# Kernel tuning notes

Measured on AMD Instinct MI355X. Metric: run time of the kernel, lower is better.

The kernel has to match this reference:

```python
import jax, jax.numpy as jnp
import numpy as np
import math

N_HEADS = 12
HEAD_DIM = 64
D_MODEL = 768
BATCH = 2
SEQ = 2048
GRID = 46  # num_patches_per_side


def _rope_1d(x, pos, dim):
    # x: (B,S,H,dim), pos: (S,) int -> rotary embedding along last dim
    inv_freq = 1.0 / (10000.0 ** (jnp.arange(0, dim, 2, dtype=jnp.float32) / dim))  # (dim/2,)
    ang = pos.astype(jnp.float32)[:, None] * inv_freq  # (S, dim/2)
    cos = jnp.concatenate([jnp.cos(ang), jnp.cos(ang)], axis=-1)[None, :, None, :]
    sin = jnp.concatenate([jnp.sin(ang), jnp.sin(ang)], axis=-1)[None, :, None, :]
    x1, x2 = jnp.split(x, 2, axis=-1)
    rot = jnp.concatenate([-x2, x1], axis=-1)
    return x * cos.astype(x.dtype) + rot * sin.astype(x.dtype)


def _rope_2d(x, row_ids, col_ids):
    # 2D RoPE: first half of head_dim rotated by row position, second half by column position
    half = x.shape[-1] // 2
    xr = _rope_1d(x[..., :half], row_ids, half)
    xc = _rope_1d(x[..., half:], col_ids, half)
    return jnp.concatenate([xr, xc], axis=-1)


def setup_inputs() -> dict:
    key = jax.random.key(0)
    ks = jax.random.split(key, 7)
    scale = 1.0 / math.sqrt(D_MODEL)
    return {
        "x": jax.random.normal(ks[0], (BATCH, SEQ, D_MODEL), dtype=jnp.float32),
        "row_ids": jax.random.randint(ks[1], (SEQ,), 0, GRID),
        "col_ids": jax.random.randint(ks[2], (SEQ,), 0, GRID),
        "Wq": jax.random.normal(ks[3], (D_MODEL, D_MODEL), dtype=jnp.float32) * scale,
        "Wk": jax.random.normal(ks[4], (D_MODEL, D_MODEL), dtype=jnp.float32) * scale,
        "Wv": jax.random.normal(ks[5], (D_MODEL, D_MODEL), dtype=jnp.float32) * scale,
        "Wo": jax.random.normal(ks[6], (D_MODEL, D_MODEL), dtype=jnp.float32) * scale,
    }


def reference(x, row_ids, col_ids, Wq, Wk, Wv, Wo):
    B, S, _ = x.shape
    # projections (nn.Linear: y = x @ W.T)
    q = (x @ Wq.T).reshape(B, S, N_HEADS, HEAD_DIM)
    k = (x @ Wk.T).reshape(B, S, N_HEADS, HEAD_DIM)
    v = (x @ Wv.T).reshape(B, S, N_HEADS, HEAD_DIM)
    q = _rope_2d(q, row_ids, col_ids)
    k = _rope_2d(k, row_ids, col_ids)
    # (B,H,S,D)
    q = q.transpose(0, 2, 1, 3)
    k = k.transpose(0, 2, 1, 3)
    v = v.transpose(0, 2, 1, 3)
    scale = 1.0 / math.sqrt(HEAD_DIM)
    scores = jnp.einsum('bhqd,bhkd->bhqk', q, k) * scale  # (B,H,S,S)
    causal = jnp.triu(jnp.ones((S, S), dtype=bool), k=1)
    scores = jnp.where(causal, -jnp.inf, scores)
    attn = jax.nn.softmax(scores, axis=-1)
    out = jnp.einsum('bhqk,bhkd->bhqd', attn, v)
    out = out.transpose(0, 2, 1, 3).reshape(B, S, D_MODEL)
    return out @ Wo.T
```

## Files before the change

kernel.cpp:

```cpp
#include <hip/hip_runtime.h>
#include <stdint.h>
#include <stddef.h>

#define DEV __device__ __forceinline__

typedef unsigned short u16;
typedef __attribute__((ext_vector_type(8))) __bf16 bf16x8;
typedef __attribute__((ext_vector_type(4))) float f32x4;
typedef __attribute__((ext_vector_type(8))) unsigned short u16x8;
typedef __attribute__((ext_vector_type(4))) unsigned short u16x4;

DEV u16 f2bf(float f) {
  uint32_t u = __builtin_bit_cast(uint32_t, f);
  u += 0x7fffu + ((u >> 16) & 1u);
  return (u16)(u >> 16);
}
DEV float bf2f(u16 h) {
  uint32_t u = ((uint32_t)h) << 16;
  return __builtin_bit_cast(float, u);
}
DEV f32x4 mfma16(bf16x8 a, bf16x8 b, f32x4 c) {
  return __builtin_amdgcn_mfma_f32_16x16x32_bf16(a, b, c, 0, 0, 0);
}
DEV void ld_lds16(const void* g, void* l) {
  __builtin_amdgcn_global_load_lds((const __attribute__((address_space(1))) void*)g,
                                   (__attribute__((address_space(3))) void*)l, 16, 0, 0);
}

#define Q_SCALE 0.18033688011112042f

__global__ __launch_bounds__(256) void k_cvt_all(const float* __restrict__ x,
                                                 const float* __restrict__ wq,
                                                 const float* __restrict__ wk,
                                                 const float* __restrict__ wv,
                                                 const float* __restrict__ wo,
                                                 u16* __restrict__ dx,
                                                 u16* __restrict__ dqkv,
                                                 u16* __restrict__ dwo) {
  const int bid = blockIdx.x;
  const float* src;
  u16* dst;
  int off;
  if (bid < 3072) {
    src = x; dst = dx; off = bid;
  } else {
    const int t = bid - 3072;
    const int w = t / 576;
    off = t - w * 576;
    src = (w == 0) ? wq : (w == 1) ? wk : (w == 2) ? wv : wo;
    dst = (w < 3) ? (dqkv + (size_t)w * 589824) : dwo;
  }
  const int i = (off * 256 + threadIdx.x) * 4;
  const float4 f = *(const float4*)(src + i);
  u16x4 o;
  o.x = f2bf(f.x); o.y = f2bf(f.y); o.z = f2bf(f.z); o.w = f2bf(f.w);
  *(u16x4*)(dst + i) = o;
}

__global__ __launch_bounds__(256) void k_gemm_qkv(const u16* __restrict__ A,
                                                  const u16* __restrict__ B,
                                                  const int* __restrict__ row_ids,
                                                  const int* __restrict__ col_ids,
                                                  u16* __restrict__ Qh,
                                                  u16* __restrict__ Kh,
                                                  u16* __restrict__ Vt) {
  const int K = 768;
  __shared__ __align__(16) u16 sA[128 * 64];
  __shared__ __align__(16) u16 sB[128 * 64];
  __shared__ int sIds[256];
  const int tid = threadIdx.x;
  const int lane = tid & 63;
  const int wid = tid >> 6;
  const int wm = wid & 1, wn = wid >> 1;
  const int col16 = lane & 15, quad = lane >> 4;
  const int rowBase = blockIdx.y * 128;
  const int colBase = blockIdx.x * 128;
  const int seg_r = lane >> 3;
  const int seg_c = lane & 7;

  f32x4 zero; zero[0] = zero[1] = zero[2] = zero[3] = 0.0f;
  f32x4 acc[4][4];
#pragma unroll
  for (int i = 0; i < 4; ++i)
#pragma unroll
    for (int j = 0; j < 4; ++j) acc[i][j] = zero;

  for (int k0 = 0; k0 < K; k0 += 64) {
#pragma unroll
    for (int c = 0; c < 4; ++c) {
      const int seg = wid * 4 + c;
      ld_lds16(A + (size_t)(rowBase + seg * 8 + seg_r) * K + k0 + seg_c * 8, sA + seg * 512);
      ld_lds16(B + (size_t)(colBase + seg * 8 + seg_r) * K + k0 + seg_c * 8, sB + seg * 512);
    }
    __syncthreads();
#pragma unroll
    for (int kk = 0; kk < 2; ++kk) {
      bf16x8 af[4], bfr[4];
#pragma unroll
      for (int t = 0; t < 4; ++t) {
        af[t]  = *(const bf16x8*)(sA + (wm * 64 + t * 16 + col16) * 64 + kk * 32 + quad * 8);
        bfr[t] = *(const bf16x8*)(sB + (wn * 64 + t * 16 + col16) * 64 + kk * 32 + quad * 8);
      }
#pragma unroll
      for (int tm = 0; tm < 4; ++tm)
#pragma unroll
        for (int tn = 0; tn < 4; ++tn)
          acc[tm][tn] = mfma16(af[tm], bfr[tn], acc[tm][tn]);
    }
    __syncthreads();
  }

  const int bx = blockIdx.x;
  const int type = bx / 6;
  const int h = (bx % 6) * 2 + wn;
  const int bb = rowBase >> 11;
  const int s0 = rowBase & 2047;
  const size_t bh = (size_t)bb * 12 + h;

  if (type < 2) {
    if (tid < 128) {
      sIds[tid] = row_ids[s0 + tid];
      sIds[128 + tid] = col_ids[s0 + tid];
    }
    __syncthreads();
    u16* dst = (type == 0) ? Qh : Kh;
    const float scl = (type == 0) ? Q_SCALE : 1.0f;
    const float invf = exp2f(-(float)col16 * 0.8304820237218406f);
#pragma unroll
    for (int tm = 0; tm < 4; ++tm)
#pragma unroll
      for (int r = 0; r < 4; ++r) {
        const int lrow = wm * 64 + tm * 16 + quad * 4 + r;
        const float aR = (float)sIds[lrow] * invf;
        const float aC = (float)sIds[128 + lrow] * invf;
        const float cR = __cosf(aR), sR = __sinf(aR);
        const float cC = __cosf(aC), sC = __sinf(aC);
        const float x1 = acc[tm][0][r], x2 = acc[tm][1][r];
        const float x3 = acc[tm][2][r], x4 = acc[tm][3][r];
        u16* p = dst + (bh * 2048 + s0 + lrow) * 64;
        p[col16]      = f2bf((x1 * cR - x2 * sR) * scl);
        p[col16 + 16] = f2bf((x2 * cR + x1 * sR) * scl);
        p[col16 + 32] = f2bf((x3 * cC - x4 * sC) * scl);
        p[col16 + 48] = f2bf((x4 * cC + x3 * sC) * scl);
      }
  } else {
#pragma unroll
    for (int tm = 0; tm < 4; ++tm)
#pragma unroll
      for (int tn = 0; tn < 4; ++tn) {
        const int d = tn * 16 + col16;
        const int srow = s0 + wm * 64 + tm * 16 + quad * 4;
        u16x4 o4;
#pragma unroll
        for (int r = 0; r < 4; ++r) o4[r] = f2bf(acc[tm][tn][r]);
        *(u16x4*)(Vt + (bh * 64 + d) * 2048 + srow) = o4;
      }
  }
}

__global__ __launch_bounds__(256, 3) void k_gemm_o(const u16* __restrict__ A,
                                                   const u16* __restrict__ B,
                                                   float* __restrict__ C,
                                                   int N, int K) {
  __shared__ __align__(16) u16 sA[64 * 72];
  __shared__ __align__(16) u16 sB[64 * 72];
  const int tid = threadIdx.x;
  const int lane = tid & 63;
  const int wid = tid >> 6;
  const int col16 = lane & 15, quad = lane >> 4;
  const int wm = wid & 1, wn = wid >> 1;
  const int rowBase = blockIdx.y * 64;
  const int colBase = blockIdx.x * 64;
  const int sr = tid >> 3;
  const int sc8 = (tid & 7) * 8;

  f32x4 zero; zero[0] = zero[1] = zero[2] = zero[3] = 0.0f;
  f32x4 acc[2][2];
  acc[0][0] = zero; acc[0][1] = zero; acc[1][0] = zero; acc[1][1] = zero;

  u16x8 ar[2], br[2];
  auto gload = [&](int k0) {
    ar[0] = *(const u16x8*)(A + (size_t)(rowBase + sr) * K + k0 + sc8);
    ar[1] = *(const u16x8*)(A + (size_t)(rowBase + 32 + sr) * K + k0 + sc8);
    br[0] = *(const u16x8*)(B + (size_t)(colBase + sr) * K + k0 + sc8);
    br[1] = *(const u16x8*)(B + (size_t)(colBase + 32 + sr) * K + k0 + sc8);
  };

  gload(0);
  for (int k0 = 0; k0 < K; k0 += 64) {
    __syncthreads();
    *(u16x8*)&sA[sr * 72 + sc8] = ar[0];
    *(u16x8*)&sA[(32 + sr) * 72 + sc8] = ar[1];
    *(u16x8*)&sB[sr * 72 + sc8] = br[0];
    *(u16x8*)&sB[(32 + sr) * 72 + sc8] = br[1];
    if (k0 + 64 < K) gload(k0 + 64);
    __syncthreads();
#pragma unroll
    for (int kk = 0; kk < 2; ++kk) {
      bf16x8 af[2], bfr[2];
#pragma unroll
      for (int t = 0; t < 2; ++t) {
        af[t]  = *(const bf16x8*)&sA[(wm * 32 + t * 16 + col16) * 72 + kk * 32 + quad * 8];
        bfr[t] = *(const bf16x8*)&sB[(wn * 32 + t * 16 + col16) * 72 + kk * 32 + quad * 8];
      }
#pragma unroll
      for (int tm = 0; tm < 2; ++tm)
#pragma unroll
        for (int tn = 0; tn < 2; ++tn)
          acc[tm][tn] = mfma16(af[tm], bfr[tn], acc[tm][tn]);
    }
  }

#pragma unroll
  for (int tm = 0; tm < 2; ++tm)
#pragma unroll
    for (int tn = 0; tn < 2; ++tn)
#pragma unroll
      for (int r = 0; r < 4; ++r) {
        const int row = rowBase + wm * 32 + tm * 16 + quad * 4 + r;
        const int col = colBase + wn * 32 + tn * 16 + col16;
        C[(size_t)row * N + col] = acc[tm][tn][r];
      }
}

__global__ __launch_bounds__(256, 3) void k_attn(const u16* __restrict__ Qh,
                                                 const u16* __restrict__ Kh,
                                                 const u16* __restrict__ Vt,
                                                 u16* __restrict__ O,
                                                 u16* __restrict__ Opart,
                                                 float* __restrict__ ml) {
  __shared__ __align__(16) u16 sK[2][64 * 72];
  __shared__ __align__(16) u16 sV[2][64 * 72];
  __shared__ __align__(16) u16 sP[4][16 * 72];
  const int tid = threadIdx.x;
  const int lane = tid & 63;
  const int wid = tid >> 6;
  const int col16 = lane & 15;
  const int quad = lane >> 4;
  const int bx = blockIdx.x;
  const int b3 = bx & 7;
  const int r_ = bx >> 3;
  const int g_ = r_ / 40;
  const int u = 39 - (r_ - g_ * 40);
  const int bh = b3 + 8 * g_;
  int qt2, c;
  if (u < 4)       { qt2 = u; c = 0; }
  else if (u < 12) { const int t = u - 4;  qt2 = 4 + (t >> 1); c = t & 1; }
  else if (u < 24) { const int t = u - 12; const int q3 = t / 3; qt2 = 8 + q3; c = t - q3 * 3; }
  else             { const int t = u - 24; qt2 = 12 + (t >> 2); c = t & 3; }
  const int nc = (qt2 >> 2) + 1;
  const int totTiles = 2 * qt2 + 2;
  const int tile0 = c * 8;
  const int ntiles = min(8, totTiles - tile0);
  const int b = bh / 12, h = bh % 12;
  const int qs0 = qt2 * 128 + wid * 16;

  const u16* Qb = Qh + (size_t)bh * (2048 * 64);
  const u16* Kb = Kh + (size_t)bh * (2048 * 64);
  const u16* Vb = Vt + (size_t)bh * (64 * 2048);

  bf16x8 bQ[2][2];
#pragma unroll
  for (int g = 0; g < 2; ++g) {
    const u16* qp = Qb + (size_t)(qs0 + g * 64 + col16) * 64 + quad * 8;
    bQ[g][0] = *(const bf16x8*)qp;
    bQ[g][1] = *(const bf16x8*)(qp + 32);
  }

  f32x4 zero; zero[0] = zero[1] = zero[2] = zero[3] = 0.0f;
  f32x4 o[2][4];
#pragma unroll
  for (int g = 0; g < 2; ++g)
#pragma unroll
    for (int i = 0; i < 4; ++i) o[g][i] = zero;
  float m_r[2] = {-1e30f, -1e30f}, l_r[2] = {0.0f, 0.0f};

  u16* sPw = &sP[wid][0];

  const int sr = tid >> 3;
  const int sc8 = (tid & 7) * 8;
  u16x8 kr[2], vr[2];
  auto gload = [&](int kt) {
#pragma unroll
    for (int i = 0; i < 2; ++i) {
      kr[i] = *(const u16x8*)(Kb + (size_t)(kt + sr + i * 32) * 64 + sc8);
      vr[i] = *(const u16x8*)(Vb + (size_t)(sr + i * 32) * 2048 + kt + sc8);
    }
  };
  auto lwrite = [&](int buf) {
#pragma unroll
    for (int i = 0; i < 2; ++i) {
      *(u16x8*)&sK[buf][(sr + i * 32) * 72 + sc8] = kr[i];
      *(u16x8*)&sV[buf][(sr + i * 32) * 72 + sc8] = vr[i];
    }
  };

  gload(tile0 * 64);
  lwrite(0);
  if (ntiles > 1) gload((tile0 + 1) * 64);
  __syncthreads();

  for (int ki = 0; ki < ntiles; ++ki) {
    const int buf = ki & 1;
    const int kt = (tile0 + ki) * 64;
    if (ki + 1 < ntiles) {
      lwrite(buf ^ 1);
      if (ki + 2 < ntiles) gload((tile0 + ki + 2) * 64);
    }
    bf16x8 ka0[4], ka1[4];
#pragma unroll
    for (int tn = 0; tn < 4; ++tn) {
      const int base = (tn * 16 + col16) * 72 + quad * 8;
      ka0[tn] = *(const bf16x8*)&sK[buf][base];
      ka1[tn] = *(const bf16x8*)&sK[buf][base + 32];
    }
    f32x4 sc[2][4];
#pragma unroll
    for (int tn = 0; tn < 4; ++tn) {
      sc[0][tn] = mfma16(ka1[tn], bQ[0][1], mfma16(ka0[tn], bQ[0][0], zero));
      sc[1][tn] = mfma16(ka1[tn], bQ[1][1], mfma16(ka0[tn], bQ[1][0], zero));
    }
    bf16x8 va0[4], va1[4];
#pragma unroll
    for (int tn = 0; tn < 4; ++tn) {
      const int base = (tn * 16 + col16) * 72 + quad * 8;
      va0[tn] = *(const bf16x8*)&sV[buf][base];
      va1[tn] = *(const bf16x8*)&sV[buf][base + 32];
    }
#pragma unroll
    for (int g = 0; g < 2; ++g) {
      const int qw = qs0 + g * 64;
      if (kt + 63 > qw) {
#pragma unroll
        for (int tn = 0; tn < 4; ++tn)
#pragma unroll
          for (int rr = 0; rr < 4; ++rr)
            if (kt + tn * 16 + quad * 4 + rr > qw + col16) sc[g][tn][rr] = -1e30f;
      }
      float vm = sc[g][0][0];
#pragma unroll
      for (int tn = 0; tn < 4; ++tn)
#pragma unroll
        for (int rr = 0; rr < 4; ++rr) vm = fmaxf(vm, sc[g][tn][rr]);
      vm = fmaxf(vm, __shfl_xor(vm, 16, 64));
      vm = fmaxf(vm, __shfl_xor(vm, 32, 64));
      if (__any(vm > m_r[g])) {
        const float mn = fmaxf(m_r[g], vm);
        const float alpha = exp2f(m_r[g] - mn);
        m_r[g] = mn;
        l_r[g] *= alpha;
#pragma unroll
        for (int t = 0; t < 4; ++t)
#pragma unroll
          for (int rr = 0; rr < 4; ++rr) o[g][t][rr] *= alpha;
      }
      const float mn = m_r[g];
      float rs = 0.0f;
#pragma unroll
      for (int tn = 0; tn < 4; ++tn)
#pragma unroll
        for (int h2 = 0; h2 < 2; ++h2) {
          const float p0 = exp2f(sc[g][tn][2 * h2] - mn);
          const float p1 = exp2f(sc[g][tn][2 * h2 + 1] - mn);
          const uint32_t u0 = __builtin_bit_cast(uint32_t, p0) & 0xffff0000u;
          const uint32_t u1 = __builtin_bit_cast(uint32_t, p1) & 0xffff0000u;
          rs += __builtin_bit_cast(float, u0) + __builtin_bit_cast(float, u1);
          ((uint32_t*)sPw)[col16 * 36 + tn * 8 + quad * 2 + h2] = u1 | (u0 >> 16);
        }
      rs += __shfl_xor(rs, 16, 64);
      rs += __shfl_xor(rs, 32, 64);
      l_r[g] += rs;
      asm volatile("s_waitcnt lgkmcnt(0)" ::: "memory");
      const bf16x8 bP0 = *(const bf16x8*)(sPw + col16 * 72 + quad * 8);
      const bf16x8 bP1 = *(const bf16x8*)(sPw + col16 * 72 + 32 + quad * 8);
#pragma unroll
      for (int tn = 0; tn < 4; ++tn)
        o[g][tn] = mfma16(va1[tn], bP1, mfma16(va0[tn], bP0, o[g][tn]));
    }
    __syncthreads();
  }

  if (nc == 1) {
#pragma unroll
    for (int g = 0; g < 2; ++g) {
      const float invl = 1.0f / l_r[g];
      const size_t row = (size_t)b * 2048 + qs0 + g * 64 + col16;
#pragma unroll
      for (int tn = 0; tn < 4; ++tn)
#pragma unroll
        for (int h2 = 0; h2 < 2; ++h2) {
          const float v0 = o[g][tn][2 * h2] * invl;
          const float v1 = o[g][tn][2 * h2 + 1] * invl;
          const uint32_t w = (uint32_t)f2bf(v0) | ((uint32_t)f2bf(v1) << 16);
          const int col = h * 64 + tn * 16 + quad * 4 + 2 * h2;
          *(uint32_t*)(O + row * 768 + col) = w;
        }
    }
  } else {
#pragma unroll
    for (int g = 0; g < 2; ++g) {
      const int prow = g * 64 + wid * 16 + col16;
      u16* op = Opart + (size_t)bx * 8192 + prow * 64;
#pragma unroll
      for (int tn = 0; tn < 4; ++tn)
#pragma unroll
        for (int h2 = 0; h2 < 2; ++h2) {
          const uint32_t w = (uint32_t)f2bf(o[g][tn][2 * h2]) |
                             ((uint32_t)f2bf(o[g][tn][2 * h2 + 1]) << 16);
          *(uint32_t*)(op + tn * 16 + quad * 4 + 2 * h2) = w;
        }
      if (quad == 0) {
        float* mlp = ml + (size_t)bx * 256;
        mlp[prow] = m_r[g];
        mlp[128 + prow] = l_r[g];
      }
    }
  }
}

__global__ __launch_bounds__(256) void k_combine(const u16* __restrict__ Opart,
                                                 const float* __restrict__ ml,
                                                 u16* __restrict__ O) {
  const int bx = blockIdx.x;
  const int bh = bx / 12;
  const int qt2 = 4 + (bx - bh * 12);
  const int b = bh / 12, h = bh % 12;
  const int nc = (qt2 >> 2) + 1;
  const int uBase = (qt2 < 8) ? (4 + 2 * (qt2 - 4))
                  : (qt2 < 12) ? (12 + 3 * (qt2 - 8))
                               : (24 + 4 * (qt2 - 12));
  const int hb3 = bh & 7, hg = bh >> 3;
  const int tid = threadIdx.x;
  const int r = tid >> 1;
  const int d0 = (tid & 1) * 32;

  int slots[4];
  for (int i = 0; i < nc; ++i)
    slots[i] = ((hg * 40 + 39 - (uBase + i)) << 3) | hb3;

  float m_i[4], w_i[4];
  float M = -1e30f;
  for (int i = 0; i < nc; ++i) {
    m_i[i] = ml[(size_t)slots[i] * 256 + r];
    M = fmaxf(M, m_i[i]);
  }
  float l = 0.0f;
  for (int i = 0; i < nc; ++i) {
    w_i[i] = exp2f(m_i[i] - M);
    l += w_i[i] * ml[(size_t)slots[i] * 256 + 128 + r];
  }
  const float invl = 1.0f / l;

  float a[32];
#pragma unroll
  for (int j = 0; j < 32; ++j) a[j] = 0.0f;
  for (int i = 0; i < nc; ++i) {
    const u16* op = Opart + (size_t)slots[i] * 8192 + r * 64 + d0;
#pragma unroll
    for (int v = 0; v < 4; ++v) {
      const u16x8 vv = *(const u16x8*)(op + v * 8);
#pragma unroll
      for (int j = 0; j < 8; ++j) a[v * 8 + j] += w_i[i] * bf2f(vv[j]);
    }
  }
  u16* dst = O + (size_t)(b * 2048 + qt2 * 128 + r) * 768 + h * 64 + d0;
#pragma unroll
  for (int v = 0; v < 4; ++v) {
    u16x8 ov;
#pragma unroll
    for (int j = 0; j < 8; ++j) ov[j] = f2bf(a[v * 8 + j] * invl);
    *(u16x8*)(dst + v * 8) = ov;
  }
}

extern "C" void kernel_launch(void* const* d_in, const int* in_sizes, int n_in,
                              void* d_out, int out_size, void* d_ws, size_t ws_size,
                              hipStream_t stream) {
  const float* x       = (const float*)d_in[0];
  const int*   row_ids = (const int*)d_in[1];
  const int*   col_ids = (const int*)d_in[2];
  const float* Wq      = (const float*)d_in[3];
  const float* Wk      = (const float*)d_in[4];
  const float* Wv      = (const float*)d_in[5];
  const float* Wo      = (const float*)d_in[6];
  float* out = (float*)d_out;

  uint8_t* w8 = (uint8_t*)d_ws;
  u16* x_bf = (u16*)(w8 + 0);
  u16* wqkv = (u16*)(w8 + 6291456);
  u16* wo   = (u16*)(w8 + 9830400);
  u16* qh   = (u16*)(w8 + 29884416);
  u16* kh   = (u16*)(w8 + 36175872);
  u16* vt   = (u16*)(w8 + 42467328);
  u16* obuf = (u16*)(w8 + 48758784);
  u16*   opart = (u16*)(w8 + 11010048);
  float* mlbuf = (float*)(w8 + 11010048 + 15728640);

  k_cvt_all<<<5376, 256, 0, stream>>>(x, Wq, Wk, Wv, Wo, x_bf, wqkv, wo);
  k_gemm_qkv<<<dim3(18, 32), 256, 0, stream>>>(x_bf, wqkv, row_ids, col_ids, qh, kh, vt);
  k_attn<<<960, 256, 0, stream>>>(qh, kh, vt, obuf, opart, mlbuf);
  k_combine<<<288, 256, 0, stream>>>(opart, mlbuf, obuf);
  k_gemm_o<<<dim3(12, 64), 256, 0, stream>>>(obuf, wo, out, 768, 768);
}
```

Baseline: 187.4 us.

## Use single-wave attention blocks loading K/V fragments directly from global memory

Attention blocks shrink from four waves covering 128 query rows to one wave covering 32 rows. The shared-memory K/V staging and block barriers go away: each wave now loads its MFMA K/V fragments straight from global memory into registers, double-buffered. The split-K chunk mapping and the combine kernel are re-indexed for the finer 32-row granularity, which raises the block count fourfold. The cost is that K/V reuse across waves through LDS is lost, so global/L2 traffic rises and fragment loads are less coalesced.

```diff
diff --git a/kernel.cpp b/kernel.cpp
--- a/kernel.cpp
+++ b/kernel.cpp
@@ -223,37 +223,33 @@
       }
 }
 
-__global__ __launch_bounds__(256, 3) void k_attn(const u16* __restrict__ Qh,
-                                                 const u16* __restrict__ Kh,
-                                                 const u16* __restrict__ Vt,
-                                                 u16* __restrict__ O,
-                                                 u16* __restrict__ Opart,
-                                                 float* __restrict__ ml) {
-  __shared__ __align__(16) u16 sK[2][64 * 72];
-  __shared__ __align__(16) u16 sV[2][64 * 72];
-  __shared__ __align__(16) u16 sP[4][16 * 72];
-  const int tid = threadIdx.x;
-  const int lane = tid & 63;
-  const int wid = tid >> 6;
+__global__ __launch_bounds__(64) void k_attn(const u16* __restrict__ Qh,
+                                             const u16* __restrict__ Kh,
+                                             const u16* __restrict__ Vt,
+                                             u16* __restrict__ O,
+                                             u16* __restrict__ Opart,
+                                             float* __restrict__ ml) {
+  __shared__ __align__(16) u16 sP[16 * 72];
+  const int lane = threadIdx.x & 63;
   const int col16 = lane & 15;
   const int quad = lane >> 4;
   const int bx = blockIdx.x;
   const int b3 = bx & 7;
-  const int r_ = bx >> 3;
-  const int g_ = r_ / 40;
-  const int u = 39 - (r_ - g_ * 40);
+  const int rest = bx >> 3;
+  const int g_ = rest / 160;
+  const int u = 159 - (rest - g_ * 160);
   const int bh = b3 + 8 * g_;
-  int qt2, c;
-  if (u < 4)       { qt2 = u; c = 0; }
-  else if (u < 12) { const int t = u - 4;  qt2 = 4 + (t >> 1); c = t & 1; }
-  else if (u < 24) { const int t = u - 12; const int q3 = t / 3; qt2 = 8 + q3; c = t - q3 * 3; }
-  else             { const int t = u - 24; qt2 = 12 + (t >> 2); c = t & 3; }
-  const int nc = (qt2 >> 2) + 1;
-  const int totTiles = 2 * qt2 + 2;
-  const int tile0 = c * 8;
-  const int ntiles = min(8, totTiles - tile0);
+  int T, c;
+  if (u < 16)      { T = u; c = 0; }
+  else if (u < 48) { const int t = u - 16; T = 16 + (t >> 1); c = t & 1; }
+  else if (u < 96) { const int t = u - 48; const int q3 = t / 3; T = 32 + q3; c = t - q3 * 3; }
+  else             { const int t = u - 96; T = 48 + (t >> 2); c = t & 3; }
+  const int kwidth = (T >> 1) + 1;
+  const int nc = (kwidth + 7) >> 3;
+  const int tlo = c * 8;
+  const int nt = min(8, kwidth - tlo);
   const int b = bh / 12, h = bh % 12;
-  const int qs0 = qt2 * 128 + wid * 16;
+  const int qb = T * 32;
 
   const u16* Qb = Qh + (size_t)bh * (2048 * 64);
   const u16* Kb = Kh + (size_t)bh * (2048 * 64);
@@ -262,7 +258,7 @@
   bf16x8 bQ[2][2];
 #pragma unroll
   for (int g = 0; g < 2; ++g) {
-    const u16* qp = Qb + (size_t)(qs0 + g * 64 + col16) * 64 + quad * 8;
+    const u16* qp = Qb + (size_t)(qb + g * 16 + col16) * 64 + quad * 8;
     bQ[g][0] = *(const bf16x8*)qp;
     bQ[g][1] = *(const bf16x8*)(qp + 32);
   }
@@ -275,61 +271,39 @@
     for (int i = 0; i < 4; ++i) o[g][i] = zero;
   float m_r[2] = {-1e30f, -1e30f}, l_r[2] = {0.0f, 0.0f};
 
-  u16* sPw = &sP[wid][0];
-
-  const int sr = tid >> 3;
-  const int sc8 = (tid & 7) * 8;
-  u16x8 kr[2], vr[2];
-  auto gload = [&](int kt) {
-#pragma unroll
-    for (int i = 0; i < 2; ++i) {
-      kr[i] = *(const u16x8*)(Kb + (size_t)(kt + sr + i * 32) * 64 + sc8);
-      vr[i] = *(const u16x8*)(Vb + (size_t)(sr + i * 32) * 2048 + kt + sc8);
+  const u16* kbase = Kb + (size_t)col16 * 64 + quad * 8;
+  const u16* vbase = Vb + (size_t)col16 * 2048 + quad * 8;
+
+  bf16x8 kf[2][8], vf[2][8];
+  auto gload = [&](int buf, int kt) {
+#pragma unroll
+    for (int tn = 0; tn < 4; ++tn) {
+      const u16* kp = kbase + (size_t)(kt + tn * 16) * 64;
+      kf[buf][tn * 2]     = *(const bf16x8*)kp;
+      kf[buf][tn * 2 + 1] = *(const bf16x8*)(kp + 32);
+      const u16* vp = vbase + (size_t)tn * (16 * 2048) + kt;
+      vf[buf][tn * 2]     = *(const bf16x8*)vp;
+      vf[buf][tn * 2 + 1] = *(const bf16x8*)(vp + 32);
     }
   };
-  auto lwrite = [&](int buf) {
-#pragma unroll
-    for (int i = 0; i < 2; ++i) {
-      *(u16x8*)&sK[buf][(sr + i * 32) * 72 + sc8] = kr[i];
-      *(u16x8*)&sV[buf][(sr + i * 32) * 72 + sc8] = vr[i];
-    }
-  };
-
-  gload(tile0 * 64);
-  lwrite(0);
-  if (ntiles > 1) gload((tile0 + 1) * 64);
-  __syncthreads();
-
-  for (int ki = 0; ki < ntiles; ++ki) {
+
+  gload(0, tlo * 64);
+  if (nt > 1) gload(1, (tlo + 1) * 64);
+
+  for (int ki = 0; ki < nt; ++ki) {
     const int buf = ki & 1;
-    const int kt = (tile0 + ki) * 64;
-    if (ki + 1 < ntiles) {
-      lwrite(buf ^ 1);
-      if (ki + 2 < ntiles) gload((tile0 + ki + 2) * 64);
-    }
-    bf16x8 ka0[4], ka1[4];
+    const int kt = (tlo + ki) * 64;
+    f32x4 sc[2][4];
 #pragma unroll
     for (int tn = 0; tn < 4; ++tn) {
-      const int base = (tn * 16 + col16) * 72 + quad * 8;
-      ka0[tn] = *(const bf16x8*)&sK[buf][base];
-      ka1[tn] = *(const bf16x8*)&sK[buf][base + 32];
-    }
-    f32x4 sc[2][4];
-#pragma unroll
-    for (int tn = 0; tn < 4; ++tn) {
-      sc[0][tn] = mfma16(ka1[tn], bQ[0][1], mfma16(ka0[tn], bQ[0][0], zero));
-      sc[1][tn] = mfma16(ka1[tn], bQ[1][1], mfma16(ka0[tn], bQ[1][0], zero));
-    }
-    bf16x8 va0[4], va1[4];
-#pragma unroll
-    for (int tn = 0; tn < 4; ++tn) {
-      const int base = (tn * 16 + col16) * 72 + quad * 8;
-      va0[tn] = *(const bf16x8*)&sV[buf][base];
-      va1[tn] = *(const bf16x8*)&sV[buf][base + 32];
+      sc[0][tn] = mfma16(kf[buf][tn * 2 + 1], bQ[0][1],
+                         mfma16(kf[buf][tn * 2], bQ[0][0], zero));
+      sc[1][tn] = mfma16(kf[buf][tn * 2 + 1], bQ[1][1],
+                         mfma16(kf[buf][tn * 2], bQ[1][0], zero));
     }
 #pragma unroll
     for (int g = 0; g < 2; ++g) {
-      const int qw = qs0 + g * 64;
+      const int qw = qb + g * 16;
       if (kt + 63 > qw) {
 #pragma unroll
         for (int tn = 0; tn < 4; ++tn)
@@ -365,26 +339,27 @@
           const uint32_t u0 = __builtin_bit_cast(uint32_t, p0) & 0xffff0000u;
           const uint32_t u1 = __builtin_bit_cast(uint32_t, p1) & 0xffff0000u;
           rs += __builtin_bit_cast(float, u0) + __builtin_bit_cast(float, u1);
-          ((uint32_t*)sPw)[col16 * 36 + tn * 8 + quad * 2 + h2] = u1 | (u0 >> 16);
+          ((uint32_t*)sP)[col16 * 36 + tn * 8 + quad * 2 + h2] = u1 | (u0 >> 16);
         }
       rs += __shfl_xor(rs, 16, 64);
       rs += __shfl_xor(rs, 32, 64);
       l_r[g] += rs;
       asm volatile("s_waitcnt lgkmcnt(0)" ::: "memory");
-      const bf16x8 bP0 = *(const bf16x8*)(sPw + col16 * 72 + quad * 8);
-      const bf16x8 bP1 = *(const bf16x8*)(sPw + col16 * 72 + 32 + quad * 8);
+      const bf16x8 bP0 = *(const bf16x8*)(sP + col16 * 72 + quad * 8);
+      const bf16x8 bP1 = *(const bf16x8*)(sP + col16 * 72 + 32 + quad * 8);
 #pragma unroll
       for (int tn = 0; tn < 4; ++tn)
-        o[g][tn] = mfma16(va1[tn], bP1, mfma16(va0[tn], bP0, o[g][tn]));
-    }
-    __syncthreads();
+        o[g][tn] = mfma16(vf[buf][tn * 2 + 1], bP1,
+                          mfma16(vf[buf][tn * 2], bP0, o[g][tn]));
+    }
+    if (ki + 2 < nt) gload(buf, kt + 128);
   }
 
   if (nc == 1) {
 #pragma unroll
     for (int g = 0; g < 2; ++g) {
       const float invl = 1.0f / l_r[g];
-      const size_t row = (size_t)b * 2048 + qs0 + g * 64 + col16;
+      const size_t row = (size_t)b * 2048 + qb + g * 16 + col16;
 #pragma unroll
       for (int tn = 0; tn < 4; ++tn)
 #pragma unroll
@@ -399,8 +374,7 @@
   } else {
 #pragma unroll
     for (int g = 0; g < 2; ++g) {
-      const int prow = g * 64 + wid * 16 + col16;
-      u16* op = Opart + (size_t)bx * 8192 + prow * 64;
+      u16* op = Opart + (size_t)bx * 2048 + (g * 16 + col16) * 64;
 #pragma unroll
       for (int tn = 0; tn < 4; ++tn)
 #pragma unroll
@@ -410,9 +384,9 @@
           *(uint32_t*)(op + tn * 16 + quad * 4 + 2 * h2) = w;
         }
       if (quad == 0) {
-        float* mlp = ml + (size_t)bx * 256;
-        mlp[prow] = m_r[g];
-        mlp[128 + prow] = l_r[g];
+        float* mlp = ml + (size_t)bx * 64;
+        mlp[g * 16 + col16] = m_r[g];
+        mlp[32 + g * 16 + col16] = l_r[g];
       }
     }
   }
@@ -422,55 +396,47 @@
                                                  const float* __restrict__ ml,
                                                  u16* __restrict__ O) {
   const int bx = blockIdx.x;
-  const int bh = bx / 12;
-  const int qt2 = 4 + (bx - bh * 12);
+  const int bh = bx / 48;
+  const int T = 16 + (bx - bh * 48);
   const int b = bh / 12, h = bh % 12;
-  const int nc = (qt2 >> 2) + 1;
-  const int uBase = (qt2 < 8) ? (4 + 2 * (qt2 - 4))
-                  : (qt2 < 12) ? (12 + 3 * (qt2 - 8))
-                               : (24 + 4 * (qt2 - 12));
-  const int hb3 = bh & 7, hg = bh >> 3;
+  const int nc = (T < 32) ? 2 : (T < 48) ? 3 : 4;
+  const int uBase = (T < 32) ? (16 + 2 * (T - 16))
+                  : (T < 48) ? (48 + 3 * (T - 32))
+                             : (96 + 4 * (T - 48));
+  const int b3 = bh & 7, g_ = bh >> 3;
   const int tid = threadIdx.x;
-  const int r = tid >> 1;
-  const int d0 = (tid & 1) * 32;
+  const int r = tid >> 3;
+  const int d0 = (tid & 7) * 8;
 
   int slots[4];
   for (int i = 0; i < nc; ++i)
-    slots[i] = ((hg * 40 + 39 - (uBase + i)) << 3) | hb3;
+    slots[i] = ((g_ * 160 + 159 - (uBase + i)) << 3) | b3;
 
   float m_i[4], w_i[4];
   float M = -1e30f;
   for (int i = 0; i < nc; ++i) {
-    m_i[i] = ml[(size_t)slots[i] * 256 + r];
+    m_i[i] = ml[(size_t)slots[i] * 64 + r];
     M = fmaxf(M, m_i[i]);
   }
   float l = 0.0f;
   for (int i = 0; i < nc; ++i) {
     w_i[i] = exp2f(m_i[i] - M);
-    l += w_i[i] * ml[(size_t)slots[i] * 256 + 128 + r];
+    l += w_i[i] * ml[(size_t)slots[i] * 64 + 32 + r];
   }
   const float invl = 1.0f / l;
 
-  float a[32];
-#pragma unroll
-  for (int j = 0; j < 32; ++j) a[j] = 0.0f;
+  float a[8];
+#pragma unroll
+  for (int j = 0; j < 8; ++j) a[j] = 0.0f;
   for (int i = 0; i < nc; ++i) {
-    const u16* op = Opart + (size_t)slots[i] * 8192 + r * 64 + d0;
-#pragma unroll
-    for (int v = 0; v < 4; ++v) {
-      const u16x8 vv = *(const u16x8*)(op + v * 8);
-#pragma unroll
-      for (int j = 0; j < 8; ++j) a[v * 8 + j] += w_i[i] * bf2f(vv[j]);
-    }
-  }
-  u16* dst = O + (size_t)(b * 2048 + qt2 * 128 + r) * 768 + h * 64 + d0;
-#pragma unroll
-  for (int v = 0; v < 4; ++v) {
-    u16x8 ov;
-#pragma unroll
-    for (int j = 0; j < 8; ++j) ov[j] = f2bf(a[v * 8 + j] * invl);
-    *(u16x8*)(dst + v * 8) = ov;
-  }
+    const u16x8 v = *(const u16x8*)(Opart + (size_t)slots[i] * 2048 + r * 64 + d0);
+#pragma unroll
+    for (int j = 0; j < 8; ++j) a[j] += w_i[i] * bf2f(v[j]);
+  }
+  u16x8 ov;
+#pragma unroll
+  for (int j = 0; j < 8; ++j) ov[j] = f2bf(a[j] * invl);
+  *(u16x8*)(O + (size_t)(b * 2048 + T * 32 + r) * 768 + h * 64 + d0) = ov;
 }
 
 extern "C" void kernel_launch(void* const* d_in, const int* in_sizes, int n_in,
@@ -498,7 +464,7 @@
 
   k_cvt_all<<<5376, 256, 0, stream>>>(x, Wq, Wk, Wv, Wo, x_bf, wqkv, wo);
   k_gemm_qkv<<<dim3(18, 32), 256, 0, stream>>>(x_bf, wqkv, row_ids, col_ids, qh, kh, vt);
-  k_attn<<<960, 256, 0, stream>>>(qh, kh, vt, obuf, opart, mlbuf);
-  k_combine<<<288, 256, 0, stream>>>(opart, mlbuf, obuf);
+  k_attn<<<3840, 64, 0, stream>>>(qh, kh, vt, obuf, opart, mlbuf);
+  k_combine<<<1152, 256, 0, stream>>>(opart, mlbuf, obuf);
   k_gemm_o<<<dim3(12, 64), 256, 0, stream>>>(obuf, wo, out, 768, 768);
 }
```

After: 325.4 us. 73.7% more time.
